# Kernel tuning notes

Hardware: AMD Instinct MI355X
Metric: run time of the kernel (lower is better)

The kernel has to match this reference:

```python
import jax, jax.numpy as jnp
import numpy as np

LN_EPS = 1e-5
BN_EPS = 1e-5


def setup_inputs() -> dict:
    key = jax.random.key(0)
    ks = jax.random.split(key, 16)
    b, n = 16, 256
    sc = 0.1
    inp = {
        "x": jax.random.normal(ks[0], (b, n, 4), jnp.float32),
        # proj: Linear(4, 64)
        "proj_w": jax.random.normal(ks[1], (4, 64), jnp.float32) * sc,
        "proj_b": jnp.zeros((64,), jnp.float32),
        # sigma_net: Linear(128,64) -> LayerNorm(64) -> ReLU -> Linear(64,1) -> Softplus
        "s_w1": jax.random.normal(ks[2], (128, 64), jnp.float32) * sc,
        "s_b1": jnp.zeros((64,), jnp.float32),
        "ln_g": jnp.ones((64,), jnp.float32),
        "ln_b": jnp.zeros((64,), jnp.float32),
        "s_w2": jax.random.normal(ks[3], (64, 1), jnp.float32) * sc,
        "s_b2": jnp.zeros((1,), jnp.float32),
        # gnn weight
        "gnn_w": jax.random.normal(ks[4], (64, 64), jnp.float32) * sc,
        # classifier: Linear(128,64) -> BatchNorm1d(64) -> ELU -> Dropout(eval) -> Linear(64,2)
        "c_w1": jax.random.normal(ks[5], (128, 64), jnp.float32) * sc,
        "c_b1": jnp.zeros((64,), jnp.float32),
        "bn_g": jnp.ones((64,), jnp.float32),
        "bn_b": jnp.zeros((64,), jnp.float32),
        "bn_mean": jnp.zeros((64,), jnp.float32),
        "bn_var": jnp.ones((64,), jnp.float32),
        "c_w2": jax.random.normal(ks[6], (64, 2), jnp.float32) * sc,
        "c_b2": jnp.zeros((2,), jnp.float32),
    }
    return inp


def reference(x, proj_w, proj_b, s_w1, s_b1, ln_g, ln_b, s_w2, s_b2,
              gnn_w, c_w1, c_b1, bn_g, bn_b, bn_mean, bn_var, c_w2, c_b2):
    # h: [b, n, 64]
    h = jax.nn.elu(x @ proj_w + proj_b)

    # sigma_net(cat([xi, xj])) == hi @ s_w1[:64] + hj @ s_w1[64:] + s_b1, broadcast pairwise
    a_i = h @ s_w1[:64]            # [b, n, 64]
    a_j = h @ s_w1[64:]            # [b, n, 64]
    pre = a_i[:, :, None, :] + a_j[:, None, :, :] + s_b1  # [b, n, n, 64]
    mu = jnp.mean(pre, axis=-1, keepdims=True)
    var = jnp.mean((pre - mu) ** 2, axis=-1, keepdims=True)
    ln = (pre - mu) * jax.lax.rsqrt(var + LN_EPS) * ln_g + ln_b
    sig_pre = jax.nn.relu(ln) @ s_w2 + s_b2               # [b, n, n, 1]
    sigmas = jax.nn.softplus(sig_pre[..., 0])             # [b, n, n]

    # squared pairwise distance via gram trick: ||hi - hj||^2
    sq = jnp.sum(h * h, axis=-1)                          # [b, n]
    gram = jnp.einsum("bid,bjd->bij", h, h)               # [b, n, n]
    d2 = jnp.maximum(sq[:, :, None] + sq[:, None, :] - 2.0 * gram, 0.0)
    adj = jnp.exp(-d2 / (2.0 * sigmas ** 2 + 1e-6))       # [b, n, n]

    h_agg = jnp.einsum("bij,bjd->bid", adj, h) @ gnn_w    # [b, n, 64]
    h_res = jax.nn.elu(h_agg + h)

    pooled = jnp.concatenate([h_res.mean(axis=1), h_res.max(axis=1)], axis=1)  # [b, 128]

    z = pooled @ c_w1 + c_b1
    z = (z - bn_mean) * jax.lax.rsqrt(bn_var + BN_EPS) * bn_g + bn_b  # BN eval mode
    z = jax.nn.elu(z)                                      # Dropout is identity in eval
    return z @ c_w2 + c_b2                                 # [b, 2]
```

## Files before the change

kernel.cpp:

```cpp
#include <hip/hip_runtime.h>
#include <math.h>

#define OFF_H      0
#define OFF_AI     262144
#define OFF_AJT    524288
#define OFF_SAI    786432
#define OFF_QAI    790528
#define OFF_SAJ    794624
#define OFF_QAJ    798720
#define OFF_SQH    802816
#define OFF_GA     806912
#define OFF_GH     1855488
#define OFF_HRES   2904064
#define OFF_BF     3166208

typedef __attribute__((ext_vector_type(8))) short bf16x8;
typedef __attribute__((ext_vector_type(4))) float f32x4;

__device__ __forceinline__ float elu_f(float x) { return x > 0.f ? x : expm1f(x); }

__device__ __forceinline__ short f2bf(float f) {
    unsigned u = __float_as_uint(f);
    unsigned r = (u + 0x7FFF + ((u >> 16) & 1)) >> 16;
    return (short)r;
}

__global__ __launch_bounds__(256) void k1_embed(
    const float* __restrict__ x,
    const float* __restrict__ proj_w, const float* __restrict__ proj_b,
    const float* __restrict__ s_w1, const float* __restrict__ s_b1,
    float* __restrict__ h, float* __restrict__ a_i, float* __restrict__ a_jT,
    short* __restrict__ ai_bf, short* __restrict__ aj_bf, short* __restrict__ h_bf,
    float* __restrict__ sa_i, float* __restrict__ qa_i,
    float* __restrict__ sa_j, float* __restrict__ qa_j,
    float* __restrict__ sqh)
{
    __shared__ float w_sh[8192];
    int tid = threadIdx.x;
    #pragma unroll
    for (int r = 0; r < 8; ++r)
        *(float4*)&w_sh[(r*256 + tid)*4] = *(const float4*)&s_w1[(r*256 + tid)*4];
    __syncthreads();

    int lane = tid & 63;
    int wave = tid >> 6;
    int row0 = blockIdx.x * 8;

    float pw0 = proj_w[lane], pw1 = proj_w[64+lane], pw2 = proj_w[128+lane],
          pw3 = proj_w[192+lane], pb = proj_b[lane], b1 = s_b1[lane];

    #pragma unroll
    for (int r = 0; r < 2; ++r) {
        int row = row0 + wave*2 + r;
        int b = row >> 8, i = row & 255;
        float4 xv = *(const float4*)&x[row*4];
        float hv = elu_f(xv.x*pw0 + xv.y*pw1 + xv.z*pw2 + xv.w*pw3 + pb);

        float ai = b1, aj = 0.f;
        #pragma unroll 8
        for (int e = 0; e < 64; ++e) {
            float he = __shfl(hv, e);
            ai = fmaf(he, w_sh[e*64 + lane], ai);
            aj = fmaf(he, w_sh[(64+e)*64 + lane], aj);
        }
        h[row*64 + lane]   = hv;
        a_i[row*64 + lane] = ai;
        a_jT[b*64*256 + lane*256 + i] = aj;
        ai_bf[row*64 + lane] = f2bf(ai);
        aj_bf[row*64 + lane] = f2bf(aj);
        h_bf [row*64 + lane] = f2bf(hv);

        float v1 = ai, v2 = ai*ai, v3 = aj, v4 = aj*aj, v5 = hv*hv;
        #pragma unroll
        for (int off = 32; off > 0; off >>= 1) {
            v1 += __shfl_xor(v1, off);
            v2 += __shfl_xor(v2, off);
            v3 += __shfl_xor(v3, off);
            v4 += __shfl_xor(v4, off);
            v5 += __shfl_xor(v5, off);
        }
        if (lane == 0) {
            sa_i[row] = v1; qa_i[row] = v2;
            sa_j[row] = v3; qa_j[row] = v4;
            sqh[row]  = v5;
        }
    }
}

__global__ __launch_bounds__(64) void kgram(
    const short* __restrict__ ai_bf, const short* __restrict__ aj_bf,
    const short* __restrict__ h_bf,
    float* __restrict__ ga, float* __restrict__ gh)
{
    int bid = blockIdx.x;
    int g = bid & 1;
    int s = (bid >> 1) & 15;
    int b = bid >> 5;
    const short* XA = (g ? h_bf : ai_bf) + b*256*64;
    const short* XB = (g ? h_bf : aj_bf) + b*256*64;
    float* G = (g ? gh : ga) + (b*256 + s*16)*256;

    int l = threadIdx.x, lo = l & 15, hi = l >> 4;

    bf16x8 a0 = *(const bf16x8*)&XA[(s*16 + lo)*64 + hi*8];
    bf16x8 a1 = *(const bf16x8*)&XA[(s*16 + lo)*64 + 32 + hi*8];

    #pragma unroll 4
    for (int jt = 0; jt < 16; ++jt) {
        bf16x8 b0 = *(const bf16x8*)&XB[(jt*16 + lo)*64 + hi*8];
        bf16x8 b1 = *(const bf16x8*)&XB[(jt*16 + lo)*64 + 32 + hi*8];
        f32x4 c = {0.f, 0.f, 0.f, 0.f};
        c = __builtin_amdgcn_mfma_f32_16x16x32_bf16(a0, b0, c, 0, 0, 0);
        c = __builtin_amdgcn_mfma_f32_16x16x32_bf16(a1, b1, c, 0, 0, 0);
        #pragma unroll
        for (int r = 0; r < 4; ++r)
            G[(hi*4 + r)*256 + jt*16 + lo] = c[r];
    }
}

__global__ __launch_bounds__(256) void k2_pair(
    const float* __restrict__ a_i, const float* __restrict__ a_jT,
    const float* __restrict__ h,
    const float* __restrict__ ga_m, const float* __restrict__ gh_m,
    const float* __restrict__ sa_i, const float* __restrict__ qa_i,
    const float* __restrict__ sa_j, const float* __restrict__ qa_j,
    const float* __restrict__ sqh,
    const float* __restrict__ ln_g, const float* __restrict__ ln_b,
    const float* __restrict__ s_w2, const float* __restrict__ s_b2,
    const float* __restrict__ gnn_w,
    float* __restrict__ h_res)
{
    int bi0 = blockIdx.x * 4;
    int b   = bi0 >> 8;
    int j   = threadIdx.x;
    int gj  = b*256 + j;

    __shared__ float aiT[64][4], hiT[64][4];
    __shared__ float gbw[64][4];
    __shared__ float sai_s[4], qai_s[4], sqi_s[4];
    __shared__ float adj_sh[256][4];
    __shared__ float part_sh[4][4][64];
    __shared__ float hagg_sh[4][64];

    {
        int i = j >> 6, d = j & 63;
        aiT[d][i] = a_i[(bi0+i)*64 + d];
        hiT[d][i] = h[(bi0+i)*64 + d];
    }
    if (j < 64) {
        gbw[j][0] = ln_g[j]; gbw[j][1] = ln_b[j]; gbw[j][2] = s_w2[j]; gbw[j][3] = 0.f;
    }
    if (j < 4) {
        sai_s[j] = sa_i[bi0+j]; qai_s[j] = qa_i[bi0+j]; sqi_s[j] = sqh[bi0+j];
    }
    float saj = sa_j[gj], qaj = qa_j[gj], sqj = sqh[gj];
    float b2  = s_b2[0];

    float ga[4], gh[4];
    #pragma unroll
    for (int i = 0; i < 4; ++i) {
        ga[i] = ga_m[(bi0+i)*256 + j];
        gh[i] = gh_m[(bi0+i)*256 + j];
    }
    __syncthreads();

    float rs4[4], nr4[4], d24[4];
    #pragma unroll
    for (int i = 0; i < 4; ++i) {
        float mu  = (sai_s[i] + saj) * (1.f/64.f);
        float pss = qai_s[i] + qaj + 2.f*ga[i];
        float var = pss * (1.f/64.f) - mu*mu;
        rs4[i] = rsqrtf(var + 1e-5f);
        nr4[i] = -mu * rs4[i];
        d24[i] = fmaxf(sqi_s[i] + sqj - 2.f*gh[i], 0.f);
    }

    const float* ajb = a_jT + b*64*256;
    float acc[4] = {0.f,0.f,0.f,0.f};
    #pragma unroll 8
    for (int d = 0; d < 64; ++d) {
        float ajd = ajb[d*256 + j];
        float4 A = *(const float4*)&aiT[d][0];
        float4 G = *(const float4*)&gbw[d][0];
        float t0 = fmaxf(fmaf(fmaf(A.x + ajd, rs4[0], nr4[0]), G.x, G.y), 0.f);
        acc[0] = fmaf(t0, G.z, acc[0]);
        float t1 = fmaxf(fmaf(fmaf(A.y + ajd, rs4[1], nr4[1]), G.x, G.y), 0.f);
        acc[1] = fmaf(t1, G.z, acc[1]);
        float t2 = fmaxf(fmaf(fmaf(A.z + ajd, rs4[2], nr4[2]), G.x, G.y), 0.f);
        acc[2] = fmaf(t2, G.z, acc[2]);
        float t3 = fmaxf(fmaf(fmaf(A.w + ajd, rs4[3], nr4[3]), G.x, G.y), 0.f);
        acc[3] = fmaf(t3, G.z, acc[3]);
    }

    {
        float4 av;
        float sp0 = acc[0] + b2;
        float sg0 = fmaxf(sp0, 0.f) + log1pf(expf(-fabsf(sp0)));
        av.x = expf(-d24[0] / (2.f*sg0*sg0 + 1e-6f));
        float sp1 = acc[1] + b2;
        float sg1 = fmaxf(sp1, 0.f) + log1pf(expf(-fabsf(sp1)));
        av.y = expf(-d24[1] / (2.f*sg1*sg1 + 1e-6f));
        float sp2 = acc[2] + b2;
        float sg2 = fmaxf(sp2, 0.f) + log1pf(expf(-fabsf(sp2)));
        av.z = expf(-d24[2] / (2.f*sg2*sg2 + 1e-6f));
        float sp3 = acc[3] + b2;
        float sg3 = fmaxf(sp3, 0.f) + log1pf(expf(-fabsf(sp3)));
        av.w = expf(-d24[3] / (2.f*sg3*sg3 + 1e-6f));
        *(float4*)&adj_sh[j][0] = av;
    }
    __syncthreads();

    int d = j & 63, q = j >> 6;
    const float* hb = h + b*256*64;
    float part[4] = {0.f,0.f,0.f,0.f};
    #pragma unroll 8
    for (int k = 0; k < 64; ++k) {
        int jj = q*64 + k;
        float hv = hb[jj*64 + d];
        float4 a4 = *(const float4*)&adj_sh[jj][0];
        part[0] = fmaf(a4.x, hv, part[0]);
        part[1] = fmaf(a4.y, hv, part[1]);
        part[2] = fmaf(a4.z, hv, part[2]);
        part[3] = fmaf(a4.w, hv, part[3]);
    }
    #pragma unroll
    for (int i = 0; i < 4; ++i) part_sh[q][i][d] = part[i];
    __syncthreads();

    {
        int i = j >> 6, dd = j & 63;
        hagg_sh[i][dd] = part_sh[0][i][dd] + part_sh[1][i][dd]
                       + part_sh[2][i][dd] + part_sh[3][i][dd];
    }
    __syncthreads();

    {
        int i = j >> 6, lane = j & 63;
        float accg = 0.f;
        #pragma unroll 8
        for (int e = 0; e < 64; ++e)
            accg = fmaf(hagg_sh[i][e], gnn_w[e*64 + lane], accg);
        h_res[(bi0+i)*64 + lane] = elu_f(accg + hiT[lane][i]);
    }
}

__global__ __launch_bounds__(256) void k4_pool_cls(
    const float* __restrict__ h_res,
    const float* __restrict__ c_w1, const float* __restrict__ c_b1,
    const float* __restrict__ bn_g, const float* __restrict__ bn_b,
    const float* __restrict__ bn_mean, const float* __restrict__ bn_var,
    const float* __restrict__ c_w2, const float* __restrict__ c_b2,
    float* __restrict__ out)
{
    int b = blockIdx.x;
    int tid = threadIdx.x;
    int d = tid & 63, q = tid >> 6;
    const float* hb = h_res + b*256*64;

    float sum = 0.f, mx = -INFINITY;
    #pragma unroll 8
    for (int k = 0; k < 64; ++k) {
        float v = hb[(q*64+k)*64 + d];
        sum += v; mx = fmaxf(mx, v);
    }
    __shared__ float sum_sh[256], max_sh[256];
    __shared__ float pm_sh[64], px_sh[64];
    sum_sh[tid] = sum; max_sh[tid] = mx;
    __syncthreads();
    if (tid < 64) {
        float tsum = sum_sh[tid] + sum_sh[64+tid] + sum_sh[128+tid] + sum_sh[192+tid];
        float tmax = fmaxf(fmaxf(max_sh[tid], max_sh[64+tid]),
                           fmaxf(max_sh[128+tid], max_sh[192+tid]));
        pm_sh[tid] = tsum * (1.f/256.f);
        px_sh[tid] = tmax;
    }
    __syncthreads();
    if (tid < 64) {
        float acc = c_b1[tid];
        #pragma unroll
        for (int e = 0; e < 64; ++e) {
            acc += pm_sh[e] * c_w1[e*64 + tid];
            acc += px_sh[e] * c_w1[(64+e)*64 + tid];
        }
        float z = (acc - bn_mean[tid]) * rsqrtf(bn_var[tid] + 1e-5f) * bn_g[tid] + bn_b[tid];
        z = elu_f(z);
        float c0 = z * c_w2[tid*2 + 0];
        float c1 = z * c_w2[tid*2 + 1];
        for (int off = 32; off > 0; off >>= 1) {
            c0 += __shfl_down(c0, off);
            c1 += __shfl_down(c1, off);
        }
        if (tid == 0) {
            out[b*2 + 0] = c0 + c_b2[0];
            out[b*2 + 1] = c1 + c_b2[1];
        }
    }
}

extern "C" void kernel_launch(void* const* d_in, const int* in_sizes, int n_in,
                              void* d_out, int out_size, void* d_ws, size_t ws_size,
                              hipStream_t stream) {
    const float* x       = (const float*)d_in[0];
    const float* proj_w  = (const float*)d_in[1];
    const float* proj_b  = (const float*)d_in[2];
    const float* s_w1    = (const float*)d_in[3];
    const float* s_b1    = (const float*)d_in[4];
    const float* ln_g    = (const float*)d_in[5];
    const float* ln_b    = (const float*)d_in[6];
    const float* s_w2    = (const float*)d_in[7];
    const float* s_b2    = (const float*)d_in[8];
    const float* gnn_w   = (const float*)d_in[9];
    const float* c_w1    = (const float*)d_in[10];
    const float* c_b1    = (const float*)d_in[11];
    const float* bn_g    = (const float*)d_in[12];
    const float* bn_b    = (const float*)d_in[13];
    const float* bn_mean = (const float*)d_in[14];
    const float* bn_var  = (const float*)d_in[15];
    const float* c_w2    = (const float*)d_in[16];
    const float* c_b2    = (const float*)d_in[17];

    float* w = (float*)d_ws;
    float* h     = w + OFF_H;
    float* a_i   = w + OFF_AI;
    float* a_jT  = w + OFF_AJT;
    float* sa_i  = w + OFF_SAI;
    float* qa_i  = w + OFF_QAI;
    float* sa_j  = w + OFF_SAJ;
    float* qa_j  = w + OFF_QAJ;
    float* sqh   = w + OFF_SQH;
    float* ga    = w + OFF_GA;
    float* gh    = w + OFF_GH;
    float* h_res = w + OFF_HRES;
    short* ai_bf = (short*)(w + OFF_BF);
    short* aj_bf = ai_bf + 262144;
    short* h_bf  = ai_bf + 524288;
    float* out   = (float*)d_out;

    k1_embed<<<512, 256, 0, stream>>>(x, proj_w, proj_b, s_w1, s_b1,
                                      h, a_i, a_jT, ai_bf, aj_bf, h_bf,
                                      sa_i, qa_i, sa_j, qa_j, sqh);
    kgram<<<512, 64, 0, stream>>>(ai_bf, aj_bf, h_bf, ga, gh);
    k2_pair<<<1024, 256, 0, stream>>>(a_i, a_jT, h, ga, gh,
                                      sa_i, qa_i, sa_j, qa_j, sqh,
                                      ln_g, ln_b, s_w2, s_b2, gnn_w, h_res);
    k4_pool_cls<<<16, 256, 0, stream>>>(h_res, c_w1, c_b1, bn_g, bn_b,
                                        bn_mean, bn_var, c_w2, c_b2, out);
}
```

Measured before the change: 52.24 us.

## Split pair kernel across j-chunks and move GNN matmul to separate kernel

The pairwise kernel now launches four blocks per 4-row tile, each handling a 64-column chunk of j with one (i,j) pair per thread. Previously each thread handled four i rows. Each block writes partial h_agg sums to a new workspace buffer, and a new k3_gnn kernel adds the four chunks, applies gnn_w and the residual ELU. The aim is more parallelism and less per-thread register work in the dominant kernel. In exchange it adds an extra launch and a global round trip for the partial aggregates.

```diff
diff --git a/kernel.cpp b/kernel.cpp
--- a/kernel.cpp
+++ b/kernel.cpp
@@ -11,8 +11,9 @@
 #define OFF_SQH    802816
 #define OFF_GA     806912
 #define OFF_GH     1855488
-#define OFF_HRES   2904064
-#define OFF_BF     3166208
+#define OFF_HAGG4  2904064
+#define OFF_HRES   3952640
+#define OFF_BF     4214784
 
 typedef __attribute__((ext_vector_type(8))) short bf16x8;
 typedef __attribute__((ext_vector_type(4))) float f32x4;
@@ -127,121 +128,107 @@
     const float* __restrict__ sqh,
     const float* __restrict__ ln_g, const float* __restrict__ ln_b,
     const float* __restrict__ s_w2, const float* __restrict__ s_b2,
-    const float* __restrict__ gnn_w,
-    float* __restrict__ h_res)
-{
-    int bi0 = blockIdx.x * 4;
-    int b   = bi0 >> 8;
-    int j   = threadIdx.x;
-    int gj  = b*256 + j;
-
-    __shared__ float aiT[64][4], hiT[64][4];
-    __shared__ float gbw[64][4];
-    __shared__ float sai_s[4], qai_s[4], sqi_s[4];
-    __shared__ float adj_sh[256][4];
-    __shared__ float part_sh[4][4][64];
-    __shared__ float hagg_sh[4][64];
+    float* __restrict__ hagg4)
+{
+    int blk  = blockIdx.x;
+    int tile = blk >> 2, ch = blk & 3;
+    int bi0  = tile * 4, b = bi0 >> 8;
+    int j0   = ch * 64;
+    int t    = threadIdx.x;
+    int i    = t >> 6, jl = t & 63;
+    int jg   = j0 + jl;
+    int gj   = b*256 + jg;
+
+    __shared__ float4 ibw[4][64];
+    __shared__ float  sai_s[4], qai_s[4], sqi_s[4];
+    __shared__ float  adj_sh[4][64];
+    __shared__ float4 part4[4][4][16];
+
+    ibw[i][jl] = make_float4(a_i[(bi0+i)*64 + jl], ln_g[jl], ln_b[jl], s_w2[jl]);
+    if (t < 4) {
+        sai_s[t] = sa_i[bi0+t]; qai_s[t] = qa_i[bi0+t]; sqi_s[t] = sqh[bi0+t];
+    }
+    float saj = sa_j[gj], qaj = qa_j[gj], sqj = sqh[gj];
+    float gav = ga_m[(bi0+i)*256 + jg];
+    float ghv = gh_m[(bi0+i)*256 + jg];
+    float b2  = s_b2[0];
+    __syncthreads();
+
+    float mu  = (sai_s[i] + saj) * (1.f/64.f);
+    float pss = qai_s[i] + qaj + 2.f*gav;
+    float var = pss * (1.f/64.f) - mu*mu;
+    float rs  = rsqrtf(var + 1e-5f);
+    float nr  = -mu * rs;
+    float d2  = fmaxf(sqi_s[i] + sqj - 2.f*ghv, 0.f);
+
+    const float* ajb = a_jT + b*64*256 + j0;
+    float acc = 0.f;
+    #pragma unroll 16
+    for (int d = 0; d < 64; ++d) {
+        float  ajd = ajb[d*256 + jl];
+        float4 B   = ibw[i][d];
+        float pre = B.x + ajd;
+        float v   = fmaf(pre, rs, nr);
+        float tt  = fmaf(v, B.y, B.z);
+        tt = fmaxf(tt, 0.f);
+        acc = fmaf(tt, B.w, acc);
+    }
 
     {
-        int i = j >> 6, d = j & 63;
-        aiT[d][i] = a_i[(bi0+i)*64 + d];
-        hiT[d][i] = h[(bi0+i)*64 + d];
-    }
-    if (j < 64) {
-        gbw[j][0] = ln_g[j]; gbw[j][1] = ln_b[j]; gbw[j][2] = s_w2[j]; gbw[j][3] = 0.f;
-    }
-    if (j < 4) {
-        sai_s[j] = sa_i[bi0+j]; qai_s[j] = qa_i[bi0+j]; sqi_s[j] = sqh[bi0+j];
-    }
-    float saj = sa_j[gj], qaj = qa_j[gj], sqj = sqh[gj];
-    float b2  = s_b2[0];
-
-    float ga[4], gh[4];
-    #pragma unroll
-    for (int i = 0; i < 4; ++i) {
-        ga[i] = ga_m[(bi0+i)*256 + j];
-        gh[i] = gh_m[(bi0+i)*256 + j];
-    }
-    __syncthreads();
-
-    float rs4[4], nr4[4], d24[4];
-    #pragma unroll
-    for (int i = 0; i < 4; ++i) {
-        float mu  = (sai_s[i] + saj) * (1.f/64.f);
-        float pss = qai_s[i] + qaj + 2.f*ga[i];
-        float var = pss * (1.f/64.f) - mu*mu;
-        rs4[i] = rsqrtf(var + 1e-5f);
-        nr4[i] = -mu * rs4[i];
-        d24[i] = fmaxf(sqi_s[i] + sqj - 2.f*gh[i], 0.f);
-    }
-
-    const float* ajb = a_jT + b*64*256;
-    float acc[4] = {0.f,0.f,0.f,0.f};
+        float sp  = acc + b2;
+        float sig = fmaxf(sp, 0.f) + log1pf(expf(-fabsf(sp)));
+        adj_sh[i][jl] = expf(-d2 / (2.f*sig*sig + 1e-6f));
+    }
+    __syncthreads();
+
+    {
+        int i2 = t >> 6, jsub = (t >> 4) & 3, dq = t & 15;
+        const float* hb = h + (b*256 + j0)*64;
+        float4 p = {0.f,0.f,0.f,0.f};
+        #pragma unroll
+        for (int k = 0; k < 16; ++k) {
+            int jj = jsub*16 + k;
+            float a = adj_sh[i2][jj];
+            float4 hv = *(const float4*)&hb[jj*64 + dq*4];
+            p.x = fmaf(a, hv.x, p.x);
+            p.y = fmaf(a, hv.y, p.y);
+            p.z = fmaf(a, hv.z, p.z);
+            p.w = fmaf(a, hv.w, p.w);
+        }
+        part4[i2][jsub][dq] = p;
+    }
+    __syncthreads();
+
+    if (t < 64) {
+        int i2 = t >> 4, dq = t & 15;
+        float4 p0 = part4[i2][0][dq], p1 = part4[i2][1][dq];
+        float4 p2 = part4[i2][2][dq], p3 = part4[i2][3][dq];
+        float4 s;
+        s.x = p0.x + p1.x + p2.x + p3.x;
+        s.y = p0.y + p1.y + p2.y + p3.y;
+        s.z = p0.z + p1.z + p2.z + p3.z;
+        s.w = p0.w + p1.w + p2.w + p3.w;
+        *(float4*)&hagg4[((size_t)ch*262144) + (size_t)(bi0 + i2)*64 + dq*4] = s;
+    }
+}
+
+__global__ __launch_bounds__(256) void k3_gnn(
+    const float* __restrict__ hagg4, const float* __restrict__ h,
+    const float* __restrict__ gnn_w, float* __restrict__ h_res)
+{
+    int lane = threadIdx.x & 63, wave = threadIdx.x >> 6;
+    int row = blockIdx.x*4 + wave;
+    __shared__ float agg_sh[4][64];
+    agg_sh[wave][lane] = hagg4[row*64 + lane]
+                       + hagg4[262144 + row*64 + lane]
+                       + hagg4[524288 + row*64 + lane]
+                       + hagg4[786432 + row*64 + lane];
+    __syncthreads();
+    float acc = 0.f;
     #pragma unroll 8
-    for (int d = 0; d < 64; ++d) {
-        float ajd = ajb[d*256 + j];
-        float4 A = *(const float4*)&aiT[d][0];
-        float4 G = *(const float4*)&gbw[d][0];
-        float t0 = fmaxf(fmaf(fmaf(A.x + ajd, rs4[0], nr4[0]), G.x, G.y), 0.f);
-        acc[0] = fmaf(t0, G.z, acc[0]);
-        float t1 = fmaxf(fmaf(fmaf(A.y + ajd, rs4[1], nr4[1]), G.x, G.y), 0.f);
-        acc[1] = fmaf(t1, G.z, acc[1]);
-        float t2 = fmaxf(fmaf(fmaf(A.z + ajd, rs4[2], nr4[2]), G.x, G.y), 0.f);
-        acc[2] = fmaf(t2, G.z, acc[2]);
-        float t3 = fmaxf(fmaf(fmaf(A.w + ajd, rs4[3], nr4[3]), G.x, G.y), 0.f);
-        acc[3] = fmaf(t3, G.z, acc[3]);
-    }
-
-    {
-        float4 av;
-        float sp0 = acc[0] + b2;
-        float sg0 = fmaxf(sp0, 0.f) + log1pf(expf(-fabsf(sp0)));
-        av.x = expf(-d24[0] / (2.f*sg0*sg0 + 1e-6f));
-        float sp1 = acc[1] + b2;
-        float sg1 = fmaxf(sp1, 0.f) + log1pf(expf(-fabsf(sp1)));
-        av.y = expf(-d24[1] / (2.f*sg1*sg1 + 1e-6f));
-        float sp2 = acc[2] + b2;
-        float sg2 = fmaxf(sp2, 0.f) + log1pf(expf(-fabsf(sp2)));
-        av.z = expf(-d24[2] / (2.f*sg2*sg2 + 1e-6f));
-        float sp3 = acc[3] + b2;
-        float sg3 = fmaxf(sp3, 0.f) + log1pf(expf(-fabsf(sp3)));
-        av.w = expf(-d24[3] / (2.f*sg3*sg3 + 1e-6f));
-        *(float4*)&adj_sh[j][0] = av;
-    }
-    __syncthreads();
-
-    int d = j & 63, q = j >> 6;
-    const float* hb = h + b*256*64;
-    float part[4] = {0.f,0.f,0.f,0.f};
-    #pragma unroll 8
-    for (int k = 0; k < 64; ++k) {
-        int jj = q*64 + k;
-        float hv = hb[jj*64 + d];
-        float4 a4 = *(const float4*)&adj_sh[jj][0];
-        part[0] = fmaf(a4.x, hv, part[0]);
-        part[1] = fmaf(a4.y, hv, part[1]);
-        part[2] = fmaf(a4.z, hv, part[2]);
-        part[3] = fmaf(a4.w, hv, part[3]);
-    }
-    #pragma unroll
-    for (int i = 0; i < 4; ++i) part_sh[q][i][d] = part[i];
-    __syncthreads();
-
-    {
-        int i = j >> 6, dd = j & 63;
-        hagg_sh[i][dd] = part_sh[0][i][dd] + part_sh[1][i][dd]
-                       + part_sh[2][i][dd] + part_sh[3][i][dd];
-    }
-    __syncthreads();
-
-    {
-        int i = j >> 6, lane = j & 63;
-        float accg = 0.f;
-        #pragma unroll 8
-        for (int e = 0; e < 64; ++e)
-            accg = fmaf(hagg_sh[i][e], gnn_w[e*64 + lane], accg);
-        h_res[(bi0+i)*64 + lane] = elu_f(accg + hiT[lane][i]);
-    }
+    for (int e = 0; e < 64; ++e)
+        acc = fmaf(agg_sh[wave][e], gnn_w[e*64 + lane], acc);
+    h_res[row*64 + lane] = elu_f(acc + h[row*64 + lane]);
 }
 
 __global__ __launch_bounds__(256) void k4_pool_cls(
@@ -330,6 +317,7 @@
     float* sqh   = w + OFF_SQH;
     float* ga    = w + OFF_GA;
     float* gh    = w + OFF_GH;
+    float* hagg4 = w + OFF_HAGG4;
     float* h_res = w + OFF_HRES;
     short* ai_bf = (short*)(w + OFF_BF);
     short* aj_bf = ai_bf + 262144;
@@ -340,9 +328,10 @@
                                       h, a_i, a_jT, ai_bf, aj_bf, h_bf,
                                       sa_i, qa_i, sa_j, qa_j, sqh);
     kgram<<<512, 64, 0, stream>>>(ai_bf, aj_bf, h_bf, ga, gh);
-    k2_pair<<<1024, 256, 0, stream>>>(a_i, a_jT, h, ga, gh,
+    k2_pair<<<4096, 256, 0, stream>>>(a_i, a_jT, h, ga, gh,
                                       sa_i, qa_i, sa_j, qa_j, sqh,
-                                      ln_g, ln_b, s_w2, s_b2, gnn_w, h_res);
+                                      ln_g, ln_b, s_w2, s_b2, hagg4);
+    k3_gnn<<<1024, 256, 0, stream>>>(hagg4, h, gnn_w, h_res);
     k4_pool_cls<<<16, 256, 0, stream>>>(h_res, c_w1, c_b1, bn_g, bn_b,
                                         bn_mean, bn_var, c_w2, c_b2, out);
 }
```

New measurement: 57.10 us. 1.09x slower.
